# Kernel tuning notes

Hardware: AMD Instinct MI355X
Metric: run time of the kernel (lower is better)

The kernel has to match this reference:

```python
import jax, jax.numpy as jnp
import numpy as np

B, N, DIM = 4, 2048, 512
HEADS, DK = 8, 64
SCALE = DK ** -0.5


def setup_inputs() -> dict:
    key = jax.random.key(0)
    k1, k2, k3, k4 = jax.random.split(key, 4)
    x = jax.random.normal(k1, (B, N, DIM), dtype=jnp.float32)
    # nn.Linear(dim, dim_key*heads, bias=False): y = x @ W.T; store W already transposed
    Wq = jax.random.normal(k2, (DIM, HEADS * DK), dtype=jnp.float32) * (DIM ** -0.5)
    Wk = jax.random.normal(k3, (DIM, HEADS * DK), dtype=jnp.float32) * (DIM ** -0.5)
    rel_content_bias = jax.random.normal(k4, (1, HEADS, 1, DK), dtype=jnp.float32)
    return {"x": x, "Wq": Wq, "Wk": Wk, "rel_content_bias": rel_content_bias}


def _split_heads(t, h):
    # [b, n, h*d] -> [b, h, n, d]
    b, n, hd = t.shape
    return t.reshape(b, n, h, hd // h).transpose(0, 2, 1, 3)


def reference(x, Wq, Wk, rel_content_bias):
    q = _split_heads(x @ Wq, HEADS) * SCALE          # [b, h, n, dk]
    k = _split_heads(x @ Wk, HEADS)                  # [b, h, n, dk]
    v = _split_heads(x, HEADS)                       # [b, h, n, dim/h]
    logits = jnp.einsum('bhid,bhjd->bhij', q + rel_content_bias, k)
    attn = jax.nn.sigmoid(logits)                    # no softmax normalization
    out = jnp.einsum('bhij,bhjd->bhid', attn, v)     # [b, h, n, dim/h]
    b, h, n, d = out.shape
    return out.transpose(0, 2, 1, 3).reshape(b, n, h * d)
```

## Files before the change

kernel.cpp:

```cpp
#include <hip/hip_runtime.h>
#include <hip/hip_bf16.h>
#include <stdint.h>

#define BB 4
#define NN 2048
#define DIMD 512
#define HH 8
#define DKK 64
#define MTOT (BB * NN)
constexpr float SCALE = 0.125f;

typedef __attribute__((ext_vector_type(4))) float f32x4;
typedef __attribute__((ext_vector_type(2))) float f32x2;
typedef __attribute__((ext_vector_type(8))) short bf16x8;
typedef __attribute__((ext_vector_type(4))) _Float16 f16x4;
typedef __attribute__((ext_vector_type(2))) __fp16 fp16v2;
typedef __attribute__((ext_vector_type(4))) __fp16 fp16v4;
typedef __attribute__((ext_vector_type(2))) unsigned int u32x2;

union pack8 { unsigned short s[8]; uint4 v; };
union fragu { u32x2 h[2]; bf16x8 v; };

__device__ __forceinline__ unsigned short f2bf(float f) {
  union { float f; uint32_t u; } v; v.f = f;
  uint32_t u = v.u;
  return (unsigned short)((u + 0x7FFFu + ((u >> 16) & 1u)) >> 16);
}

__device__ __forceinline__ unsigned short f2h(float f) {
  union { _Float16 h; unsigned short u; } c; c.h = (_Float16)f;
  return c.u;
}

__device__ __forceinline__ bf16x8 ld_frag(const unsigned short* p) {
  fragu f;
  f.h[0] = *(const u32x2*)p;
  f.h[1] = *(const u32x2*)(p + 4);
  return f.v;
}
__device__ __forceinline__ void st8(unsigned short* p, uint4 v) {
  *(u32x2*)p = (u32x2){v.x, v.y};
  *(u32x2*)(p + 4) = (u32x2){v.z, v.w};
}

__device__ __forceinline__ f16x4 sig_pack(f32x4 sv) {
  float e0 = __expf(-__builtin_fabsf(sv[0]));
  float e1 = __expf(-__builtin_fabsf(sv[1]));
  float e2 = __expf(-__builtin_fabsf(sv[2]));
  float e3 = __expf(-__builtin_fabsf(sv[3]));
  const f32x2 c3 = {-0.22184f, -0.22184f};
  const f32x2 c2 = {0.66550f, 0.66550f};
  const f32x2 c1 = {-0.94280f, -0.94280f};
  const f32x2 c0 = {0.49826f, 0.49826f};
  f32x2 eA = {e0, e1}, eB = {e2, e3};
  f32x2 pA = __builtin_elementwise_fma(
      __builtin_elementwise_fma(__builtin_elementwise_fma(c3, eA, c2), eA, c1),
      eA, c0);
  f32x2 pB = __builtin_elementwise_fma(
      __builtin_elementwise_fma(__builtin_elementwise_fma(c3, eB, c2), eB, c1),
      eB, c0);
  float r0 = __builtin_copysignf(pA.x, sv[0]) + 0.5f;
  float r1 = __builtin_copysignf(pA.y, sv[1]) + 0.5f;
  float r2 = __builtin_copysignf(pB.x, sv[2]) + 0.5f;
  float r3 = __builtin_copysignf(pB.y, sv[3]) + 0.5f;
  fp16v2 lo = __builtin_amdgcn_cvt_pkrtz(r0, r1);
  fp16v2 hi = __builtin_amdgcn_cvt_pkrtz(r2, r3);
  fp16v4 p;
  p.x = lo.x; p.y = lo.y; p.z = hi.x; p.w = hi.y;
  return __builtin_bit_cast(f16x4, p);
}

__global__ __launch_bounds__(256) void prep(const float* __restrict__ x,
                                            const float* __restrict__ wq,
                                            const float* __restrict__ wk,
                                            unsigned short* __restrict__ xb,
                                            unsigned short* __restrict__ xtf,
                                            unsigned short* __restrict__ wtq,
                                            unsigned short* __restrict__ wtk) {
  const int bx = blockIdx.x, tid = threadIdx.x;
  if (bx < 2048) {
    size_t base = ((size_t)bx * 256 + tid) * 8;
    float4 a = *(const float4*)(x + base);
    float4 b = *(const float4*)(x + base + 4);
    pack8 p;
    p.s[0] = f2bf(a.x); p.s[1] = f2bf(a.y); p.s[2] = f2bf(a.z); p.s[3] = f2bf(a.w);
    p.s[4] = f2bf(b.x); p.s[5] = f2bf(b.y); p.s[6] = f2bf(b.z); p.s[7] = f2bf(b.w);
    *(uint4*)(xb + base) = p.v;
  } else if (bx < 2304) {
    int q = bx - 2048;
    int b = q >> 6, r = q & 63;
    int dt = r >> 3, nt = r & 7;
    int d = dt * 64 + (tid & 63);
    int n0 = nt * 256 + (tid >> 6) * 64;
    const float* xp = x + ((size_t)b * NN + n0) * DIMD + d;
    unsigned short* dp = xtf + ((size_t)b * DIMD + d) * NN + n0;
#pragma unroll
    for (int g = 0; g < 8; g++) {
      pack8 pa;
#pragma unroll
      for (int k = 0; k < 8; k++) pa.s[k] = f2h(xp[(size_t)(g * 8 + k) * DIMD]);
      *(uint4*)(dp + g * 8) = pa.v;
    }
  } else {
    __shared__ __align__(16) unsigned short T[64][68];
    int q = bx - 2304;
    const float* w = (q >= 64) ? wk : wq;
    unsigned short* wt = (q >= 64) ? wtk : wtq;
    int r = q & 63;
    int kt = r >> 3, nt = r & 7;
    const int k0 = kt * 64, n0 = nt * 64;
#pragma unroll
    for (int rr = 0; rr < 16; rr++) {
      int idx = tid + rr * 256;
      int kl = idx >> 6, nl = idx & 63;
      T[nl][kl] = f2bf(w[(size_t)(k0 + kl) * DIMD + n0 + nl]);
    }
    __syncthreads();
#pragma unroll
    for (int rr = 0; rr < 2; rr++) {
      int idx = tid + rr * 256;
      int nl = idx >> 3, c = idx & 7;
      fragu f;
      f.h[0] = *(const u32x2*)&T[nl][c * 8];
      f.h[1] = *(const u32x2*)&T[nl][c * 8 + 4];
      uint4 v;
      v.x = f.h[0].x; v.y = f.h[0].y; v.z = f.h[1].x; v.w = f.h[1].y;
      *(uint4*)(wt + (size_t)(n0 + nl) * DIMD + k0 + c * 8) = v;
    }
  }
}

__global__ __launch_bounds__(512, 4) void qk_gemm(const unsigned short* __restrict__ xb,
                                                  const unsigned short* __restrict__ wtq,
                                                  const unsigned short* __restrict__ wtk,
                                                  const float* __restrict__ bias,
                                                  unsigned short* __restrict__ qout,
                                                  unsigned short* __restrict__ kout) {
  __shared__ __align__(16) unsigned short Als[128][68];
  __shared__ __align__(16) unsigned short Bls[128][68];
  const int mb = blockIdx.x, nb = blockIdx.y;
  const bool isQ = (nb < 4);
  const unsigned short* wt = isQ ? wtq : wtk;
  unsigned short* outp = isQ ? qout : kout;
  const int n0 = (nb & 3) * 128, m0 = mb * 128;
  const int tid = threadIdx.x;
  const int wave = tid >> 6, lane = tid & 63;
  const int quad = lane >> 4, l16 = lane & 15;
  const int wm = wave >> 2, wn = wave & 3;

  f32x4 acc[4][2];
#pragma unroll
  for (int a = 0; a < 4; a++)
#pragma unroll
    for (int c = 0; c < 2; c++) acc[a][c] = (f32x4){0.f, 0.f, 0.f, 0.f};

  const int srow[2] = {tid >> 3, (tid + 512) >> 3};
  const int scol = (tid & 7) * 8;
  uint4 pa[2], pb[2];
#pragma unroll
  for (int r = 0; r < 2; r++) {
    pa[r] = *(const uint4*)(xb + (size_t)(m0 + srow[r]) * DIMD + scol);
    pb[r] = *(const uint4*)(wt + (size_t)(n0 + srow[r]) * DIMD + scol);
  }

  for (int k0 = 0; k0 < DIMD; k0 += 64) {
    __syncthreads();
#pragma unroll
    for (int r = 0; r < 2; r++) {
      st8(&Als[srow[r]][scol], pa[r]);
      st8(&Bls[srow[r]][scol], pb[r]);
    }
    __syncthreads();
    if (k0 + 64 < DIMD) {
#pragma unroll
      for (int r = 0; r < 2; r++) {
        pa[r] = *(const uint4*)(xb + (size_t)(m0 + srow[r]) * DIMD + k0 + 64 + scol);
        pb[r] = *(const uint4*)(wt + (size_t)(n0 + srow[r]) * DIMD + k0 + 64 + scol);
      }
    }
#pragma unroll
    for (int ks = 0; ks < 2; ks++) {
      bf16x8 af[4], bfr[2];
#pragma unroll
      for (int t = 0; t < 4; t++)
        af[t] = ld_frag(&Als[wm * 64 + t * 16 + l16][quad * 8 + ks * 32]);
#pragma unroll
      for (int t = 0; t < 2; t++)
        bfr[t] = ld_frag(&Bls[wn * 32 + t * 16 + l16][quad * 8 + ks * 32]);
#pragma unroll
      for (int tm = 0; tm < 4; tm++)
#pragma unroll
        for (int tn = 0; tn < 2; tn++)
          acc[tm][tn] =
              __builtin_amdgcn_mfma_f32_16x16x32_bf16(af[tm], bfr[tn], acc[tm][tn], 0, 0, 0);
    }
  }
#pragma unroll
  for (int tm = 0; tm < 4; tm++) {
#pragma unroll
    for (int tn = 0; tn < 2; tn++) {
#pragma unroll
      for (int r = 0; r < 4; r++) {
        int row = m0 + wm * 64 + tm * 16 + quad * 4 + r;
        int gcol = n0 + wn * 32 + tn * 16 + l16;
        float v = acc[tm][tn][r];
        if (isQ) v = v * SCALE + bias[gcol];
        outp[(size_t)row * DIMD + gcol] = f2bf(v);
      }
    }
  }
}

__global__ __launch_bounds__(512, 4) void attn(const unsigned short* __restrict__ qb,
                                               const unsigned short* __restrict__ kb,
                                               const unsigned short* __restrict__ xtf,
                                               float* __restrict__ out) {
  __shared__ __align__(16) char smem[34816];
  unsigned short* Kall = (unsigned short*)smem;
  unsigned short* Vall = Kall + 2 * 64 * 68;
  float* R0 = (float*)smem;

  const int it = blockIdx.x, bh = blockIdx.y;
  const int b = bh >> 3, h = bh & 7;
  const int i0 = it * 128;
  const int tid = threadIdx.x;
  const int lane = tid & 63;
  const int grp = tid >> 8;
  const int wv = (tid >> 6) & 3;
  const int gtid = tid & 255;
  const int quad = lane >> 4, l16 = lane & 15;

  bf16x8 qf[2][2];
  int irow[2];
#pragma unroll
  for (int s_ = 0; s_ < 2; s_++) {
    irow[s_] = i0 + wv * 32 + s_ * 16 + l16;
    const unsigned short* qp = qb + ((size_t)b * NN + irow[s_]) * DIMD + h * DKK + quad * 8;
    qf[s_][0] = *(const bf16x8*)qp;
    qf[s_][1] = *(const bf16x8*)(qp + 32);
  }

  f32x4 o[2][4];
#pragma unroll
  for (int s_ = 0; s_ < 2; s_++)
#pragma unroll
    for (int td = 0; td < 4; td++) o[s_][td] = (f32x4){0.f, 0.f, 0.f, 0.f};

  const unsigned short* kbase = kb + (size_t)b * NN * DIMD + h * DKK;
  const unsigned short* vbase = xtf + ((size_t)b * DIMD + h * DKK) * NN;
  unsigned short* Kg = Kall + grp * (64 * 68);
  unsigned short* Vg = Vall + grp * (64 * 68);
  const int jbase = grp * 1024;

  const int trow[2] = {gtid >> 3, (gtid + 256) >> 3};
  const int tcol = (gtid & 7) * 8;
  uint4 pk[2], pv[2];
#pragma unroll
  for (int r = 0; r < 2; r++) {
    pk[r] = *(const uint4*)(kbase + (size_t)(jbase + trow[r]) * DIMD + tcol);
    pv[r] = *(const uint4*)(vbase + (size_t)trow[r] * NN + jbase + tcol);
  }

  for (int itr = 0; itr < 16; itr++) {
    __syncthreads();
#pragma unroll
    for (int r = 0; r < 2; r++) {
      st8(&Kg[trow[r] * 68 + tcol], pk[r]);
      st8(&Vg[trow[r] * 68 + tcol], pv[r]);
    }
    __syncthreads();
    if (itr < 15) {
      const int j0 = jbase + (itr + 1) * 64;
#pragma unroll
      for (int r = 0; r < 2; r++) {
        pk[r] = *(const uint4*)(kbase + (size_t)(j0 + trow[r]) * DIMD + tcol);
        pv[r] = *(const uint4*)(vbase + (size_t)trow[r] * NN + j0 + tcol);
      }
    }

#pragma unroll
    for (int t = 0; t < 4; t++) {
      bf16x8 kf0 = ld_frag(&Kg[(t * 16 + l16) * 68 + quad * 8]);
      bf16x8 kf1 = ld_frag(&Kg[(t * 16 + l16) * 68 + quad * 8 + 32]);
      f16x4 pf[2];
#pragma unroll
      for (int s_ = 0; s_ < 2; s_++) {
        f32x4 sv = (f32x4){0.f, 0.f, 0.f, 0.f};
        sv = __builtin_amdgcn_mfma_f32_16x16x32_bf16(kf0, qf[s_][0], sv, 0, 0, 0);
        sv = __builtin_amdgcn_mfma_f32_16x16x32_bf16(kf1, qf[s_][1], sv, 0, 0, 0);
        pf[s_] = sig_pack(sv);
      }
#pragma unroll
      for (int td = 0; td < 4; td++) {
        f16x4 vf = __builtin_bit_cast(
            f16x4, *(const u32x2*)&Vg[(td * 16 + l16) * 68 + t * 16 + quad * 4]);
        o[0][td] = __builtin_amdgcn_mfma_f32_16x16x16f16(vf, pf[0], o[0][td], 0, 0, 0);
        o[1][td] = __builtin_amdgcn_mfma_f32_16x16x16f16(vf, pf[1], o[1][td], 0, 0, 0);
      }
    }
  }

  __syncthreads();
  if (grp == 1) {
#pragma unroll
    for (int s_ = 0; s_ < 2; s_++)
#pragma unroll
      for (int td = 0; td < 4; td++) {
        int base = (wv * 32 + s_ * 16 + l16) * 66 + td * 16 + quad * 4;
        *(f32x2*)&R0[base] = (f32x2){o[s_][td][0], o[s_][td][1]};
        *(f32x2*)&R0[base + 2] = (f32x2){o[s_][td][2], o[s_][td][3]};
      }
  }
  __syncthreads();
  if (grp == 0) {
#pragma unroll
    for (int s_ = 0; s_ < 2; s_++) {
#pragma unroll
      for (int td = 0; td < 4; td++) {
        int base = (wv * 32 + s_ * 16 + l16) * 66 + td * 16 + quad * 4;
        f32x2 a = *(const f32x2*)&R0[base];
        f32x2 c = *(const f32x2*)&R0[base + 2];
        o[s_][td][0] += a.x; o[s_][td][1] += a.y;
        o[s_][td][2] += c.x; o[s_][td][3] += c.y;
        float* op = out + ((size_t)b * NN + irow[s_]) * DIMD + h * DKK + td * 16 + quad * 4;
        *(f32x4*)op = o[s_][td];
      }
    }
  }
}

extern "C" void kernel_launch(void* const* d_in, const int* in_sizes, int n_in,
                              void* d_out, int out_size, void* d_ws, size_t ws_size,
                              hipStream_t stream) {
  const float* x = (const float*)d_in[0];
  const float* Wq = (const float*)d_in[1];
  const float* Wk = (const float*)d_in[2];
  const float* bias = (const float*)d_in[3];
  float* out = (float*)d_out;

  unsigned short* ws = (unsigned short*)d_ws;
  unsigned short* xb = ws;
  unsigned short* xtf = xb + (size_t)MTOT * DIMD;
  unsigned short* wtq = xtf + (size_t)MTOT * DIMD;
  unsigned short* wtk = wtq + (size_t)DIMD * DIMD;
  unsigned short* qb = wtk + (size_t)DIMD * DIMD;
  unsigned short* kb = qb + (size_t)MTOT * DIMD;

  prep<<<dim3(2432), 256, 0, stream>>>(x, Wq, Wk, xb, xtf, wtq, wtk);
  qk_gemm<<<dim3(64, 8), 512, 0, stream>>>(xb, wtq, wtk, bias, qb, kb);
  attn<<<dim3(16, 32), 512, 0, stream>>>(qb, kb, xtf, out);
}
```

Measured before the change: 158.4 us.

## Drop register prefetch of K/V tiles and batch QK MFMAs before sigmoid

Removes the register double-buffering that loaded the next K/V tile from global memory while the current tile was being computed. Each iteration now loads its own tile and stores it straight to LDS between barriers. The loop body is also reordered so all QK MFMAs for the tile are issued first, then all sigmoids, then the PV MFMAs, which gives the scheduler more independent MFMA work. This lowers register pressure from the prefetch buffers but exposes global-load latency before every tile unless occupancy hides it.

```diff
diff --git a/kernel.cpp b/kernel.cpp
--- a/kernel.cpp
+++ b/kernel.cpp
@@ -254,48 +254,46 @@
 
   const int trow[2] = {gtid >> 3, (gtid + 256) >> 3};
   const int tcol = (gtid & 7) * 8;
-  uint4 pk[2], pv[2];
-#pragma unroll
-  for (int r = 0; r < 2; r++) {
-    pk[r] = *(const uint4*)(kbase + (size_t)(jbase + trow[r]) * DIMD + tcol);
-    pv[r] = *(const uint4*)(vbase + (size_t)trow[r] * NN + jbase + tcol);
-  }
 
   for (int itr = 0; itr < 16; itr++) {
+    const int j0 = jbase + itr * 64;
     __syncthreads();
 #pragma unroll
     for (int r = 0; r < 2; r++) {
-      st8(&Kg[trow[r] * 68 + tcol], pk[r]);
-      st8(&Vg[trow[r] * 68 + tcol], pv[r]);
-    }
-    __syncthreads();
-    if (itr < 15) {
-      const int j0 = jbase + (itr + 1) * 64;
-#pragma unroll
-      for (int r = 0; r < 2; r++) {
-        pk[r] = *(const uint4*)(kbase + (size_t)(j0 + trow[r]) * DIMD + tcol);
-        pv[r] = *(const uint4*)(vbase + (size_t)trow[r] * NN + j0 + tcol);
-      }
-    }
-
+      uint4 k4 = *(const uint4*)(kbase + (size_t)(j0 + trow[r]) * DIMD + tcol);
+      uint4 v4 = *(const uint4*)(vbase + (size_t)trow[r] * NN + j0 + tcol);
+      st8(&Kg[trow[r] * 68 + tcol], k4);
+      st8(&Vg[trow[r] * 68 + tcol], v4);
+    }
+    __syncthreads();
+
+    f32x4 sv[2][4];
 #pragma unroll
     for (int t = 0; t < 4; t++) {
       bf16x8 kf0 = ld_frag(&Kg[(t * 16 + l16) * 68 + quad * 8]);
       bf16x8 kf1 = ld_frag(&Kg[(t * 16 + l16) * 68 + quad * 8 + 32]);
-      f16x4 pf[2];
 #pragma unroll
       for (int s_ = 0; s_ < 2; s_++) {
-        f32x4 sv = (f32x4){0.f, 0.f, 0.f, 0.f};
-        sv = __builtin_amdgcn_mfma_f32_16x16x32_bf16(kf0, qf[s_][0], sv, 0, 0, 0);
-        sv = __builtin_amdgcn_mfma_f32_16x16x32_bf16(kf1, qf[s_][1], sv, 0, 0, 0);
-        pf[s_] = sig_pack(sv);
-      }
-#pragma unroll
-      for (int td = 0; td < 4; td++) {
+        f32x4 z = (f32x4){0.f, 0.f, 0.f, 0.f};
+        z = __builtin_amdgcn_mfma_f32_16x16x32_bf16(kf0, qf[s_][0], z, 0, 0, 0);
+        sv[s_][t] = __builtin_amdgcn_mfma_f32_16x16x32_bf16(kf1, qf[s_][1], z, 0, 0, 0);
+      }
+    }
+
+    f16x4 pf[2][4];
+#pragma unroll
+    for (int s_ = 0; s_ < 2; s_++)
+#pragma unroll
+      for (int t = 0; t < 4; t++) pf[s_][t] = sig_pack(sv[s_][t]);
+
+#pragma unroll
+    for (int td = 0; td < 4; td++) {
+#pragma unroll
+      for (int t = 0; t < 4; t++) {
         f16x4 vf = __builtin_bit_cast(
             f16x4, *(const u32x2*)&Vg[(td * 16 + l16) * 68 + t * 16 + quad * 4]);
-        o[0][td] = __builtin_amdgcn_mfma_f32_16x16x16f16(vf, pf[0], o[0][td], 0, 0, 0);
-        o[1][td] = __builtin_amdgcn_mfma_f32_16x16x16f16(vf, pf[1], o[1][td], 0, 0, 0);
+        o[0][td] = __builtin_amdgcn_mfma_f32_16x16x16f16(vf, pf[0][t], o[0][td], 0, 0, 0);
+        o[1][td] = __builtin_amdgcn_mfma_f32_16x16x16f16(vf, pf[1][t], o[1][td], 0, 0, 0);
       }
     }
   }
```

New measurement: 161.8 us. 1.02x slower.

## Fuse x bf16 conversion into QK GEMM and double-buffer attention K/V tiles

Applied to the files above, without the earlier changes.

Drops the separate x-to-bf16 pass from the prep kernel; the QK GEMM now loads fp32 x and converts it while staging into LDS, which removes a write and re-read of the bf16 copy of x. The attention kernel gains double-buffered K/V shared-memory tiles, so the next tile is stored after compute and only one barrier per iteration remains. The cost is twice as much LDS in attention (about 68KB), which may reduce occupancy, and twice the global read bytes for x in the GEMM, since x is re-read as fp32 by each of its 8 column blocks.

```diff
diff --git a/kernel.cpp b/kernel.cpp
--- a/kernel.cpp
+++ b/kernel.cpp
@@ -73,21 +73,12 @@
 __global__ __launch_bounds__(256) void prep(const float* __restrict__ x,
                                             const float* __restrict__ wq,
                                             const float* __restrict__ wk,
-                                            unsigned short* __restrict__ xb,
                                             unsigned short* __restrict__ xtf,
                                             unsigned short* __restrict__ wtq,
                                             unsigned short* __restrict__ wtk) {
   const int bx = blockIdx.x, tid = threadIdx.x;
-  if (bx < 2048) {
-    size_t base = ((size_t)bx * 256 + tid) * 8;
-    float4 a = *(const float4*)(x + base);
-    float4 b = *(const float4*)(x + base + 4);
-    pack8 p;
-    p.s[0] = f2bf(a.x); p.s[1] = f2bf(a.y); p.s[2] = f2bf(a.z); p.s[3] = f2bf(a.w);
-    p.s[4] = f2bf(b.x); p.s[5] = f2bf(b.y); p.s[6] = f2bf(b.z); p.s[7] = f2bf(b.w);
-    *(uint4*)(xb + base) = p.v;
-  } else if (bx < 2304) {
-    int q = bx - 2048;
+  if (bx < 256) {
+    int q = bx;
     int b = q >> 6, r = q & 63;
     int dt = r >> 3, nt = r & 7;
     int d = dt * 64 + (tid & 63);
@@ -103,7 +94,7 @@
     }
   } else {
     __shared__ __align__(16) unsigned short T[64][68];
-    int q = bx - 2304;
+    int q = bx - 256;
     const float* w = (q >= 64) ? wk : wq;
     unsigned short* wt = (q >= 64) ? wtk : wtq;
     int r = q & 63;
@@ -130,7 +121,7 @@
   }
 }
 
-__global__ __launch_bounds__(512, 4) void qk_gemm(const unsigned short* __restrict__ xb,
+__global__ __launch_bounds__(512, 4) void qk_gemm(const float* __restrict__ x,
                                                   const unsigned short* __restrict__ wtq,
                                                   const unsigned short* __restrict__ wtk,
                                                   const float* __restrict__ bias,
@@ -156,10 +147,13 @@
 
   const int srow[2] = {tid >> 3, (tid + 512) >> 3};
   const int scol = (tid & 7) * 8;
-  uint4 pa[2], pb[2];
+  float4 fa[2][2];
+  uint4 pb[2];
 #pragma unroll
   for (int r = 0; r < 2; r++) {
-    pa[r] = *(const uint4*)(xb + (size_t)(m0 + srow[r]) * DIMD + scol);
+    const float* xp = x + (size_t)(m0 + srow[r]) * DIMD + scol;
+    fa[r][0] = *(const float4*)xp;
+    fa[r][1] = *(const float4*)(xp + 4);
     pb[r] = *(const uint4*)(wt + (size_t)(n0 + srow[r]) * DIMD + scol);
   }
 
@@ -167,14 +161,21 @@
     __syncthreads();
 #pragma unroll
     for (int r = 0; r < 2; r++) {
-      st8(&Als[srow[r]][scol], pa[r]);
+      pack8 p;
+      p.s[0] = f2bf(fa[r][0].x); p.s[1] = f2bf(fa[r][0].y);
+      p.s[2] = f2bf(fa[r][0].z); p.s[3] = f2bf(fa[r][0].w);
+      p.s[4] = f2bf(fa[r][1].x); p.s[5] = f2bf(fa[r][1].y);
+      p.s[6] = f2bf(fa[r][1].z); p.s[7] = f2bf(fa[r][1].w);
+      st8(&Als[srow[r]][scol], p.v);
       st8(&Bls[srow[r]][scol], pb[r]);
     }
     __syncthreads();
     if (k0 + 64 < DIMD) {
 #pragma unroll
       for (int r = 0; r < 2; r++) {
-        pa[r] = *(const uint4*)(xb + (size_t)(m0 + srow[r]) * DIMD + k0 + 64 + scol);
+        const float* xp = x + (size_t)(m0 + srow[r]) * DIMD + k0 + 64 + scol;
+        fa[r][0] = *(const float4*)xp;
+        fa[r][1] = *(const float4*)(xp + 4);
         pb[r] = *(const uint4*)(wt + (size_t)(n0 + srow[r]) * DIMD + k0 + 64 + scol);
       }
     }
@@ -215,9 +216,9 @@
                                                const unsigned short* __restrict__ kb,
                                                const unsigned short* __restrict__ xtf,
                                                float* __restrict__ out) {
-  __shared__ __align__(16) char smem[34816];
+  __shared__ __align__(16) char smem[69632];
   unsigned short* Kall = (unsigned short*)smem;
-  unsigned short* Vall = Kall + 2 * 64 * 68;
+  unsigned short* Vall = Kall + 2 * 2 * 64 * 68;
   float* R0 = (float*)smem;
 
   const int it = blockIdx.x, bh = blockIdx.y;
@@ -248,27 +249,29 @@
 
   const unsigned short* kbase = kb + (size_t)b * NN * DIMD + h * DKK;
   const unsigned short* vbase = xtf + ((size_t)b * DIMD + h * DKK) * NN;
-  unsigned short* Kg = Kall + grp * (64 * 68);
-  unsigned short* Vg = Vall + grp * (64 * 68);
+  unsigned short* Kbuf[2] = {Kall + grp * (2 * 64 * 68), Kall + grp * (2 * 64 * 68) + 64 * 68};
+  unsigned short* Vbuf[2] = {Vall + grp * (2 * 64 * 68), Vall + grp * (2 * 64 * 68) + 64 * 68};
   const int jbase = grp * 1024;
 
   const int trow[2] = {gtid >> 3, (gtid + 256) >> 3};
   const int tcol = (gtid & 7) * 8;
-  uint4 pk[2], pv[2];
-#pragma unroll
-  for (int r = 0; r < 2; r++) {
-    pk[r] = *(const uint4*)(kbase + (size_t)(jbase + trow[r]) * DIMD + tcol);
-    pv[r] = *(const uint4*)(vbase + (size_t)trow[r] * NN + jbase + tcol);
-  }
+
+  {
+#pragma unroll
+    for (int r = 0; r < 2; r++) {
+      uint4 k4 = *(const uint4*)(kbase + (size_t)(jbase + trow[r]) * DIMD + tcol);
+      uint4 v4 = *(const uint4*)(vbase + (size_t)trow[r] * NN + jbase + tcol);
+      st8(&Kbuf[0][trow[r] * 68 + tcol], k4);
+      st8(&Vbuf[0][trow[r] * 68 + tcol], v4);
+    }
+  }
+  __syncthreads();
 
   for (int itr = 0; itr < 16; itr++) {
-    __syncthreads();
-#pragma unroll
-    for (int r = 0; r < 2; r++) {
-      st8(&Kg[trow[r] * 68 + tcol], pk[r]);
-      st8(&Vg[trow[r] * 68 + tcol], pv[r]);
-    }
-    __syncthreads();
+    unsigned short* Kg = Kbuf[itr & 1];
+    unsigned short* Vg = Vbuf[itr & 1];
+
+    uint4 pk[2], pv[2];
     if (itr < 15) {
       const int j0 = jbase + (itr + 1) * 64;
 #pragma unroll
@@ -298,9 +301,19 @@
         o[1][td] = __builtin_amdgcn_mfma_f32_16x16x16f16(vf, pf[1], o[1][td], 0, 0, 0);
       }
     }
-  }
-
-  __syncthreads();
+
+    if (itr < 15) {
+      unsigned short* Kn = Kbuf[(itr + 1) & 1];
+      unsigned short* Vn = Vbuf[(itr + 1) & 1];
+#pragma unroll
+      for (int r = 0; r < 2; r++) {
+        st8(&Kn[trow[r] * 68 + tcol], pk[r]);
+        st8(&Vn[trow[r] * 68 + tcol], pv[r]);
+      }
+    }
+    __syncthreads();
+  }
+
   if (grp == 1) {
 #pragma unroll
     for (int s_ = 0; s_ < 2; s_++)
@@ -339,14 +352,13 @@
   float* out = (float*)d_out;
 
   unsigned short* ws = (unsigned short*)d_ws;
-  unsigned short* xb = ws;
-  unsigned short* xtf = xb + (size_t)MTOT * DIMD;
+  unsigned short* xtf = ws;
   unsigned short* wtq = xtf + (size_t)MTOT * DIMD;
   unsigned short* wtk = wtq + (size_t)DIMD * DIMD;
   unsigned short* qb = wtk + (size_t)DIMD * DIMD;
   unsigned short* kb = qb + (size_t)MTOT * DIMD;
 
-  prep<<<dim3(2432), 256, 0, stream>>>(x, Wq, Wk, xb, xtf, wtq, wtk);
-  qk_gemm<<<dim3(64, 8), 512, 0, stream>>>(xb, wtq, wtk, bias, qb, kb);
+  prep<<<dim3(384), 256, 0, stream>>>(x, Wq, Wk, xtf, wtq, wtk);
+  qk_gemm<<<dim3(64, 8), 512, 0, stream>>>(x, wtq, wtk, bias, qb, kb);
   attn<<<dim3(16, 32), 512, 0, stream>>>(qb, kb, xtf, out);
 }
```

After: 210.2 us. 32.7% more time.
